# Kernel optimization log

Measured on AMD Instinct MI355X. Metric: run time of the kernel, lower is better.

Reference implementation:

```python
import jax, jax.numpy as jnp
import numpy as np
from jax import lax

FEATURE_NUM = 16
FILTERS = 64
BATCH = 64
WINDOW = 5
T = 2048
SECTORS = 11
D = 256          # embedding dim / number of quantization buckets
DA = 64
VOCAB = 100000
L = T - 3 * WINDOW + 3  # 2036, length after conv->maxpool->conv (all valid, stride 1)
BN_EPS = 1e-5


def _conv1d(x, w):
    # x: [N, C, W], w: [O, I, K], valid padding, stride 1
    return lax.conv_general_dilated(x, w, (1,), 'VALID', dimension_numbers=('NCH', 'OIH', 'NCH'))


def setup_inputs() -> dict:
    key = jax.random.key(0)
    ks = jax.random.split(key, 9)
    x = jax.random.normal(ks[0], (BATCH, 2 * FEATURE_NUM, T), jnp.float32)
    conv1_w = jax.random.normal(ks[1], (FILTERS, 2 * FEATURE_NUM, WINDOW), jnp.float32) * 0.1
    conv1_b = jnp.zeros((FILTERS,), jnp.float32)
    bn_gamma = jnp.ones((FILTERS,), jnp.float32)
    bn_beta = jnp.zeros((FILTERS,), jnp.float32)
    conv2_w = jax.random.normal(ks[2], (1, FILTERS, WINDOW), jnp.float32) * 0.1
    conv2_b = jnp.zeros((1,), jnp.float32)
    emb = jax.random.normal(ks[3], (VOCAB, D), jnp.float32)
    W1 = jax.random.normal(ks[4], (DA, L), jnp.float32)
    W2 = jax.random.normal(ks[5], (DA, 1), jnp.float32)
    lin_w = jax.random.normal(ks[6], (SECTORS, D), jnp.float32) * 0.05
    lin_b = jnp.zeros((SECTORS,), jnp.float32)
    return {'x': x, 'conv1_w': conv1_w, 'conv1_b': conv1_b, 'bn_gamma': bn_gamma,
            'bn_beta': bn_beta, 'conv2_w': conv2_w, 'conv2_b': conv2_b, 'emb': emb,
            'W1': W1, 'W2': W2, 'lin_w': lin_w, 'lin_b': lin_b}


def reference(x, conv1_w, conv1_b, bn_gamma, bn_beta, conv2_w, conv2_b, emb, W1, W2, lin_w, lin_b):
    # conv1 (valid) -> maxpool(k=WINDOW, s=1) -> batchnorm (train-mode batch stats) -> conv2 -> relu
    h = _conv1d(x, conv1_w) + conv1_b[None, :, None]                     # [B, F, T-W+1]
    h = lax.reduce_window(h, -jnp.inf, lax.max, (1, 1, WINDOW), (1, 1, 1), 'VALID')
    mu = jnp.mean(h, axis=(0, 2), keepdims=True)
    var = jnp.mean((h - mu) ** 2, axis=(0, 2), keepdims=True)            # biased, as torch BN train
    h = (h - mu) * lax.rsqrt(var + BN_EPS) * bn_gamma[None, :, None] + bn_beta[None, :, None]
    h = jax.nn.relu(_conv1d(h, conv2_w) + conv2_b[None, :, None])        # [B, 1, L]
    c = jax.nn.sigmoid(h[:, 0, :])                                       # [B, L] in (0,1)
    # embedding_generate: first j with c <= (j+1)/D  <=>  j = ceil(c*D) - 1
    idx = jnp.clip(jnp.ceil(c * D).astype(jnp.int32) - 1, 0, D - 1)      # [B, L]
    e = emb[idx]                                                         # [B, L, D]
    # per-sample attention: A = W2^T tanh(W1 @ out), batched as einsums
    t = jnp.tanh(jnp.einsum('al,bld->bad', W1, e))                       # [B, DA, D]
    A = jnp.einsum('a,bad->bd', W2[:, 0], t)                             # [B, D]
    att = jax.nn.softmax(jnp.einsum('bld,bd->bl', e, A), axis=1)         # [B, L]
    scores = A @ lin_w.T + lin_b                                         # [B, SECTORS]
    return att, scores
```

## Files before the change

### kernel.cpp

```cpp
#include <hip/hip_runtime.h>
#include <hip/hip_bf16.h>
#include <math.h>

#define BATCH 64
#define CIN   32
#define TIN   2048
#define FILT  64
#define WIN   5
#define TP1   2044
#define TP2   2040
#define LOUT  2036
#define DEMB  256
#define DA    64
#define NSEC  11
#define NC    4
#define CS    509
#define TILE_T 252

__global__ __launch_bounds__(256) void k_prep(
    const float* __restrict__ W1, const float* __restrict__ emb,
    const float* __restrict__ w1, float* __restrict__ w1t,
    float* __restrict__ embT, float* __restrict__ w1r, int* __restrict__ count) {
  __shared__ float tl[64 * 65];
  int bk = blockIdx.x;
  const int tid = threadIdx.x;
  if (bk < 64) { count[bk * 256 + tid] = 0; return; }
  bk -= 64;
  if (bk < 32) {
    const int l0 = bk * 64;
    const int lc = tid & 63, rq = tid >> 6;
    for (int a = rq; a < 64; a += 4)
      tl[a * 65 + lc] = (l0 + lc < LOUT) ? W1[a * LOUT + l0 + lc] : 0.f;
    __syncthreads();
    for (int lp = rq; lp < 64; lp += 4)
      if (l0 + lp < LOUT) w1t[(l0 + lp) * 64 + lc] = tl[lc * 65 + lp];
    return;
  }
  bk -= 32;
  if (bk < 16) {
    const int j0 = (bk & 3) * 64, d0 = (bk >> 2) * 64;
    const int c = tid & 63, rq = tid >> 6;
    for (int j = rq; j < 64; j += 4) tl[j * 65 + c] = emb[(j0 + j) * DEMB + d0 + c];
    __syncthreads();
    for (int d = rq; d < 64; d += 4) embT[(d0 + d) * DEMB + j0 + c] = tl[c * 65 + d];
    return;
  }
  bk -= 16;
  {
    int i = bk * 256 + tid;
    int c = i / 320, r = i - c * 320, f = r / 5, k = r - f * 5;
    w1r[i] = w1[f * (CIN * WIN) + c * WIN + k];
  }
}

__global__ __launch_bounds__(256) void k_conv1pool(
    const float* __restrict__ x, const float* __restrict__ w1r,
    const float* __restrict__ b1, float* __restrict__ h2,
    float* __restrict__ bnps, float* __restrict__ bnpq) {
  __shared__ float xl[CIN * 264];
  const int b   = blockIdx.y;
  const int t0  = blockIdx.x * TILE_T;
  const int tid = threadIdx.x;

  for (int i = tid; i < CIN * 264; i += 256) {
    int c = i / 264, o = i - c * 264;
    int gt = t0 + o;
    float v = 0.f;
    if (o < 260 && gt < TIN) v = x[(b * CIN + c) * TIN + gt];
    xl[i] = v;
  }
  __syncthreads();

  const int tg  = tid & 63;
  const int tb  = tg * 4;
  const int wf0 = __builtin_amdgcn_readfirstlane((int)blockIdx.z * 32 + (tid >> 6) * 8);

  float acc[8][4];
#pragma unroll
  for (int ff = 0; ff < 8; ++ff) {
    float bias = b1[wf0 + ff];
    acc[ff][0] = bias; acc[ff][1] = bias; acc[ff][2] = bias; acc[ff][3] = bias;
  }

  for (int c = 0; c < CIN; ++c) {
    float4 xa  = *(const float4*)&xl[c * 264 + tb];
    float4 xb4 = *(const float4*)&xl[c * 264 + tb + 4];
    float xw[8] = {xa.x, xa.y, xa.z, xa.w, xb4.x, xb4.y, xb4.z, xb4.w};
    const float* wr = w1r + c * 320 + wf0 * 5;
#pragma unroll
    for (int ff = 0; ff < 8; ++ff) {
#pragma unroll
      for (int k = 0; k < WIN; ++k) {
        float wv = wr[ff * 5 + k];
        acc[ff][0] = fmaf(xw[k + 0], wv, acc[ff][0]);
        acc[ff][1] = fmaf(xw[k + 1], wv, acc[ff][1]);
        acc[ff][2] = fmaf(xw[k + 2], wv, acc[ff][2]);
        acc[ff][3] = fmaf(xw[k + 3], wv, acc[ff][3]);
      }
    }
  }

  const bool rowvalid = (tg < 63);
  const int blk = b * 9 + blockIdx.x;
#pragma unroll
  for (int ff = 0; ff < 8; ++ff) {
    float n0 = __shfl_down(acc[ff][0], 1);
    float n1 = __shfl_down(acc[ff][1], 1);
    float n2 = __shfl_down(acc[ff][2], 1);
    float n3 = __shfl_down(acc[ff][3], 1);
    float h[8] = {acc[ff][0], acc[ff][1], acc[ff][2], acc[ff][3], n0, n1, n2, n3};
    float o0 = fmaxf(fmaxf(fmaxf(h[0], h[1]), fmaxf(h[2], h[3])), h[4]);
    float o1 = fmaxf(fmaxf(fmaxf(h[1], h[2]), fmaxf(h[3], h[4])), h[5]);
    float o2 = fmaxf(fmaxf(fmaxf(h[2], h[3]), fmaxf(h[4], h[5])), h[6]);
    float o3 = fmaxf(fmaxf(fmaxf(h[3], h[4]), fmaxf(h[5], h[6])), h[7]);
    const int f = wf0 + ff;
    float s = 0.f, q = 0.f;
    const int t2b = t0 + tb;
    if (rowvalid && (t2b + 3 < TP2)) {
      *(float4*)&h2[(b * FILT + f) * TP2 + t2b] = make_float4(o0, o1, o2, o3);
      s = o0 + o1 + o2 + o3;
      q = o0 * o0 + o1 * o1 + o2 * o2 + o3 * o3;
    } else if (rowvalid) {
      float ov[4] = {o0, o1, o2, o3};
#pragma unroll
      for (int j = 0; j < 4; ++j) {
        int t2 = t2b + j;
        if (t2 < TP2) { h2[(b * FILT + f) * TP2 + t2] = ov[j]; s += ov[j]; q += ov[j] * ov[j]; }
      }
    }
#pragma unroll
    for (int off = 32; off > 0; off >>= 1) {
      s += __shfl_down(s, off);
      q += __shfl_down(q, off);
    }
    if (tg == 0) { bnps[blk * FILT + f] = s; bnpq[blk * FILT + f] = q; }
  }
}

__global__ __launch_bounds__(256) void k_bnfin(
    const float* __restrict__ bnps, const float* __restrict__ bnpq,
    const float* __restrict__ gamma, const float* __restrict__ beta,
    const float* __restrict__ w2, const float* __restrict__ b2,
    double* __restrict__ ws2, double* __restrict__ c0p) {
  __shared__ double ls[4 * 64], lq[4 * 64];
  const int tid = threadIdx.x;
  const int f = tid & 63, g = tid >> 6;
  double s = 0.0, q = 0.0;
  for (int blk = g; blk < 576; blk += 4) {
    s += (double)bnps[blk * FILT + f];
    q += (double)bnpq[blk * FILT + f];
  }
  ls[g * 64 + f] = s; lq[g * 64 + f] = q;
  __syncthreads();
  if (tid < 64) {
    s = ls[tid] + ls[64 + tid] + ls[128 + tid] + ls[192 + tid];
    q = lq[tid] + lq[64 + tid] + lq[128 + tid] + lq[192 + tid];
    const double N = (double)(BATCH * TP2);
    double mu  = s / N;
    double var = q / N - mu * mu;
    double sc  = (double)gamma[tid] / sqrt(var + 1e-5);
    double sh  = (double)beta[tid] - mu * sc;
    double wsum = 0.0;
#pragma unroll
    for (int k = 0; k < WIN; ++k) {
      double wv = (double)w2[tid * WIN + k];
      ws2[tid * WIN + k] = sc * wv;
      wsum += wv;
    }
    double part = sh * wsum;
#pragma unroll
    for (int off = 32; off > 0; off >>= 1) part += __shfl_down(part, off);
    if (tid == 0) c0p[0] = part + (double)b2[0];
  }
}

__global__ __launch_bounds__(256) void k_conv2(
    const float* __restrict__ h2, const double* __restrict__ ws2,
    const double* __restrict__ c0p, int* __restrict__ idxp, int* __restrict__ count) {
  __shared__ float hl[FILT * 260];
  __shared__ int hist[DEMB];
  const int b = blockIdx.y;
  const int t0 = blockIdx.x * 256;
  const int tid = threadIdx.x;
  for (int i = tid; i < FILT * 260; i += 256) {
    int f = i / 260, o = i - f * 260;
    int gt = t0 + o;
    hl[i] = (gt < TP2) ? h2[(b * FILT + f) * TP2 + gt] : 0.f;
  }
  hist[tid] = 0;
  __syncthreads();
  const int t = t0 + tid;
  if (t < LOUT) {
    double z = c0p[0];
    for (int f = 0; f < FILT; ++f) {
      const double* wr = ws2 + f * WIN;
      z = fma((double)hl[f * 260 + tid + 0], wr[0], z);
      z = fma((double)hl[f * 260 + tid + 1], wr[1], z);
      z = fma((double)hl[f * 260 + tid + 2], wr[2], z);
      z = fma((double)hl[f * 260 + tid + 3], wr[3], z);
      z = fma((double)hl[f * 260 + tid + 4], wr[4], z);
    }
    z = z > 0.0 ? z : 0.0;
    double c = 1.0 / (1.0 + exp(-z));
    int iv = (int)ceil(c * 256.0) - 1;
    iv = min(max(iv, 0), DEMB - 1);
    idxp[b * LOUT + t] = iv;
    atomicAdd(&hist[iv], 1);
  }
  __syncthreads();
  atomicAdd(&count[b * DEMB + tid], hist[tid]);
}

__global__ __launch_bounds__(256) void k_sbuild(
    const int* __restrict__ idxp, const float* __restrict__ w1t,
    float* __restrict__ Sg) {
  __shared__ float S[DA * 257];
  __shared__ int il[512];
  const int b = blockIdx.y, ch = blockIdx.x;
  const int tid = threadIdx.x;
  for (int i = tid; i < DA * 257; i += 256) S[i] = 0.f;
  const int l0 = ch * CS;
  for (int i = tid; i < CS; i += 256) il[i] = idxp[b * LOUT + l0 + i];
  __syncthreads();
  const int a = tid & 63, w = tid >> 6;
#pragma unroll 4
  for (int li = w; li < CS; li += 4) {
    int j = il[li];
    float v = w1t[(l0 + li) * DA + a];
    atomicAdd(&S[a * 257 + j], v);
  }
  __syncthreads();
  for (int i = tid; i < DA * DEMB; i += 256) {
    int aa = i >> 8, j = i & 255;
    Sg[((b * NC + ch) * DA + aa) * DEMB + j] = S[aa * 257 + j];
  }
}

__global__ __launch_bounds__(256) void k_gemmA(
    const float* __restrict__ Sg, const float* __restrict__ emb,
    const float* __restrict__ W2, float* __restrict__ Avec) {
  __shared__ float Al[16 * 64];
  __shared__ float Bl[16 * 64];
  __shared__ float red[16 * 64];
  const int b = blockIdx.x, c0 = blockIdx.y * 64;
  const int tid = threadIdx.x;
  const int tx = tid & 15, ty = tid >> 4;
  const int sa = tid >> 2, skq = (tid & 3) * 4;
  const int bk = tid >> 4, bseg = tid & 15;
  float acc[4][4] = {{0}};

  for (int kc = 0; kc < 16; ++kc) {
    const int kb = kc * 16;
    float4 v0 = *(const float4*)&Sg[((b * NC + 0) * DA + sa) * DEMB + kb + skq];
    float4 v1 = *(const float4*)&Sg[((b * NC + 1) * DA + sa) * DEMB + kb + skq];
    float4 v2 = *(const float4*)&Sg[((b * NC + 2) * DA + sa) * DEMB + kb + skq];
    float4 v3 = *(const float4*)&Sg[((b * NC + 3) * DA + sa) * DEMB + kb + skq];
    float4 sv = make_float4(v0.x + v1.x + v2.x + v3.x, v0.y + v1.y + v2.y + v3.y,
                            v0.z + v1.z + v2.z + v3.z, v0.w + v1.w + v2.w + v3.w);
    Al[(skq + 0) * 64 + sa] = sv.x;
    Al[(skq + 1) * 64 + sa] = sv.y;
    Al[(skq + 2) * 64 + sa] = sv.z;
    Al[(skq + 3) * 64 + sa] = sv.w;
    float4 e4 = *(const float4*)&emb[(kb + bk) * DEMB + c0 + bseg * 4];
    *(float4*)&Bl[bk * 64 + bseg * 4] = e4;
    __syncthreads();
#pragma unroll
    for (int k = 0; k < 16; ++k) {
      float4 av = *(const float4*)&Al[k * 64 + ty * 4];
      float4 bv = *(const float4*)&Bl[k * 64 + tx * 4];
      acc[0][0] = fmaf(av.x, bv.x, acc[0][0]); acc[0][1] = fmaf(av.x, bv.y, acc[0][1]);
      acc[0][2] = fmaf(av.x, bv.z, acc[0][2]); acc[0][3] = fmaf(av.x, bv.w, acc[0][3]);
      acc[1][0] = fmaf(av.y, bv.x, acc[1][0]); acc[1][1] = fmaf(av.y, bv.y, acc[1][1]);
      acc[1][2] = fmaf(av.y, bv.z, acc[1][2]); acc[1][3] = fmaf(av.y, bv.w, acc[1][3]);
      acc[2][0] = fmaf(av.z, bv.x, acc[2][0]); acc[2][1] = fmaf(av.z, bv.y, acc[2][1]);
      acc[2][2] = fmaf(av.z, bv.z, acc[2][2]); acc[2][3] = fmaf(av.z, bv.w, acc[2][3]);
      acc[3][0] = fmaf(av.w, bv.x, acc[3][0]); acc[3][1] = fmaf(av.w, bv.y, acc[3][1]);
      acc[3][2] = fmaf(av.w, bv.z, acc[3][2]); acc[3][3] = fmaf(av.w, bv.w, acc[3][3]);
    }
    __syncthreads();
  }
  float cs[4] = {0.f, 0.f, 0.f, 0.f};
#pragma unroll
  for (int r = 0; r < 4; ++r) {
    float wv = W2[ty * 4 + r];
#pragma unroll
    for (int j = 0; j < 4; ++j) cs[j] += tanhf(acc[r][j]) * wv;
  }
#pragma unroll
  for (int j = 0; j < 4; ++j) red[ty * 64 + tx * 4 + j] = cs[j];
  __syncthreads();
  if (tid < 64) {
    float s = 0.f;
#pragma unroll
    for (int q = 0; q < 16; ++q) s += red[q * 64 + tid];
    Avec[b * DEMB + c0 + tid] = s;
  }
}

__global__ __launch_bounds__(256) void k_att(
    const float* __restrict__ Avec, const float* __restrict__ embT,
    const int* __restrict__ count, const float* __restrict__ linw,
    const float* __restrict__ linb, const int* __restrict__ idxp,
    float* __restrict__ att, float* __restrict__ scores) {
  __shared__ float Al[DEMB];
  __shared__ float pl[DEMB];
  __shared__ float scratch[4];
  const int b = blockIdx.x, j = threadIdx.x;
  Al[j] = Avec[b * DEMB + j];
  __syncthreads();
  float dot = 0.f;
  for (int d = 0; d < DEMB; ++d) dot = fmaf(embT[d * DEMB + j], Al[d], dot);
  const int cnt = count[b * DEMB + j];
  float v = (cnt > 0) ? dot : -3.4e38f;
#pragma unroll
  for (int off = 32; off > 0; off >>= 1) v = fmaxf(v, __shfl_down(v, off));
  if ((j & 63) == 0) scratch[j >> 6] = v;
  __syncthreads();
  const float m = fmaxf(fmaxf(scratch[0], scratch[1]), fmaxf(scratch[2], scratch[3]));
  __syncthreads();
  float e = (cnt > 0) ? expf(dot - m) : 0.f;
  float zs = e * (float)cnt;
#pragma unroll
  for (int off = 32; off > 0; off >>= 1) zs += __shfl_down(zs, off);
  if ((j & 63) == 0) scratch[j >> 6] = zs;
  __syncthreads();
  const float Z = scratch[0] + scratch[1] + scratch[2] + scratch[3];
  pl[j] = (cnt > 0) ? e / Z : 0.f;
  __syncthreads();
  for (int l = j; l < LOUT; l += 256)
    att[b * LOUT + l] = pl[idxp[b * LOUT + l]];
  for (int s = 0; s < NSEC; ++s) {
    __syncthreads();
    float part = Al[j] * linw[s * DEMB + j];
#pragma unroll
    for (int off = 32; off > 0; off >>= 1) part += __shfl_down(part, off);
    if ((j & 63) == 0) scratch[j >> 6] = part;
    __syncthreads();
    if (j == 0)
      scores[b * NSEC + s] = scratch[0] + scratch[1] + scratch[2] + scratch[3] + linb[s];
  }
}

extern "C" void kernel_launch(void* const* d_in, const int* in_sizes, int n_in,
                              void* d_out, int out_size, void* d_ws, size_t ws_size,
                              hipStream_t stream) {
  const float* x      = (const float*)d_in[0];
  const float* w1     = (const float*)d_in[1];
  const float* b1     = (const float*)d_in[2];
  const float* gamma  = (const float*)d_in[3];
  const float* beta   = (const float*)d_in[4];
  const float* w2     = (const float*)d_in[5];
  const float* b2     = (const float*)d_in[6];
  const float* emb    = (const float*)d_in[7];
  const float* W1     = (const float*)d_in[8];
  const float* W2     = (const float*)d_in[9];
  const float* linw   = (const float*)d_in[10];
  const float* linb   = (const float*)d_in[11];

  char* ws = (char*)d_ws;
  int*    count = (int*)   (ws + 0);
  double* ws2   = (double*)(ws + 65536);
  double* c0p   = (double*)(ws + 68096);
  float*  bnps  = (float*) (ws + 68608);
  float*  bnpq  = (float*) (ws + 216064);
  int*    idxp  = (int*)   (ws + 363520);
  float*  w1t   = (float*) (ws + 884736);
  float*  embT  = (float*) (ws + 1405952);
  float*  Avec  = (float*) (ws + 1668096);
  float*  w1r   = (float*) (ws + 1733632);
  float*  h2    = (float*) (ws + 1774592);
  float*  Sg    = (float*) (ws + 35197952);

  float* att_out    = (float*)d_out;
  float* scores_out = (float*)d_out + BATCH * LOUT;

  k_prep<<<dim3(152), 256, 0, stream>>>(W1, emb, w1, w1t, embT, w1r, count);
  k_conv1pool<<<dim3(9, 64, 2), 256, 0, stream>>>(x, w1r, b1, h2, bnps, bnpq);
  k_bnfin<<<dim3(1), 256, 0, stream>>>(bnps, bnpq, gamma, beta, w2, b2, ws2, c0p);
  k_conv2<<<dim3(8, 64), 256, 0, stream>>>(h2, ws2, c0p, idxp, count);
  k_sbuild<<<dim3(NC, 64), 256, 0, stream>>>(idxp, w1t, Sg);
  k_gemmA<<<dim3(64, 4), 256, 0, stream>>>(Sg, emb, W2, Avec);
  k_att<<<dim3(64), 256, 0, stream>>>(Avec, embT, count, linw, linb, idxp,
                                      att_out, scores_out);
}
```

Measured before the change: 377.0 us.

## Stage conv1 weights in LDS and read input directly from global memory

The conv1+maxpool kernel no longer stages the input tile in shared memory. Each thread now loads its eight input values straight from global memory with float4 reads and a bounds-checked fallback at the edge. The per-block half of the reordered conv1 weights is staged in LDS instead and read as float4 vectors into registers, replacing the scalar global weight loads. This trades input reuse through LDS for cached global reads of overlapping windows, and the 40-element weight array in registers raises register pressure. Index arithmetic is also widened to size_t.

```diff
diff --git a/kernel.cpp b/kernel.cpp
--- a/kernel.cpp
+++ b/kernel.cpp
@@ -57,23 +57,22 @@
     const float* __restrict__ x, const float* __restrict__ w1r,
     const float* __restrict__ b1, float* __restrict__ h2,
     float* __restrict__ bnps, float* __restrict__ bnpq) {
-  __shared__ float xl[CIN * 264];
+  __shared__ float wl[CIN * 160];
   const int b   = blockIdx.y;
   const int t0  = blockIdx.x * TILE_T;
   const int tid = threadIdx.x;
-
-  for (int i = tid; i < CIN * 264; i += 256) {
-    int c = i / 264, o = i - c * 264;
-    int gt = t0 + o;
-    float v = 0.f;
-    if (o < 260 && gt < TIN) v = x[(b * CIN + c) * TIN + gt];
-    xl[i] = v;
-  }
-  __syncthreads();
-
-  const int tg  = tid & 63;
-  const int tb  = tg * 4;
-  const int wf0 = __builtin_amdgcn_readfirstlane((int)blockIdx.z * 32 + (tid >> 6) * 8);
+  const int z   = blockIdx.z;
+
+  for (int i = tid; i < CIN * 160; i += 256) {
+    int c = i / 160, r = i - c * 160;
+    wl[i] = w1r[c * 320 + z * 160 + r];
+  }
+  __syncthreads();
+
+  const int tg   = tid & 63;
+  const int tb   = tg * 4;
+  const int wv40 = (tid >> 6) * 40;
+  const int wf0  = __builtin_amdgcn_readfirstlane(z * 32 + (tid >> 6) * 8);
 
   float acc[8][4];
 #pragma unroll
@@ -82,16 +81,35 @@
     acc[ff][0] = bias; acc[ff][1] = bias; acc[ff][2] = bias; acc[ff][3] = bias;
   }
 
+  const float* xrow = x + (size_t)b * CIN * TIN + t0 + tb;
+  const bool safe = (t0 + tb + 8) <= TIN;
+
   for (int c = 0; c < CIN; ++c) {
-    float4 xa  = *(const float4*)&xl[c * 264 + tb];
-    float4 xb4 = *(const float4*)&xl[c * 264 + tb + 4];
-    float xw[8] = {xa.x, xa.y, xa.z, xa.w, xb4.x, xb4.y, xb4.z, xb4.w};
-    const float* wr = w1r + c * 320 + wf0 * 5;
+    float xw[8];
+    if (safe) {
+      float4 xa = *(const float4*)(xrow + c * TIN);
+      float4 xb = *(const float4*)(xrow + c * TIN + 4);
+      xw[0] = xa.x; xw[1] = xa.y; xw[2] = xa.z; xw[3] = xa.w;
+      xw[4] = xb.x; xw[5] = xb.y; xw[6] = xb.z; xw[7] = xb.w;
+    } else {
+#pragma unroll
+      for (int j = 0; j < 8; ++j) {
+        int gt = t0 + tb + j;
+        xw[j] = (gt < TIN) ? xrow[c * TIN + j] : 0.f;
+      }
+    }
+    float wa[40];
+#pragma unroll
+    for (int q = 0; q < 10; ++q) {
+      float4 wq = *(const float4*)&wl[c * 160 + wv40 + q * 4];
+      wa[q * 4 + 0] = wq.x; wa[q * 4 + 1] = wq.y;
+      wa[q * 4 + 2] = wq.z; wa[q * 4 + 3] = wq.w;
+    }
 #pragma unroll
     for (int ff = 0; ff < 8; ++ff) {
 #pragma unroll
       for (int k = 0; k < WIN; ++k) {
-        float wv = wr[ff * 5 + k];
+        float wv = wa[ff * 5 + k];
         acc[ff][0] = fmaf(xw[k + 0], wv, acc[ff][0]);
         acc[ff][1] = fmaf(xw[k + 1], wv, acc[ff][1]);
         acc[ff][2] = fmaf(xw[k + 2], wv, acc[ff][2]);
@@ -117,7 +135,7 @@
     float s = 0.f, q = 0.f;
     const int t2b = t0 + tb;
     if (rowvalid && (t2b + 3 < TP2)) {
-      *(float4*)&h2[(b * FILT + f) * TP2 + t2b] = make_float4(o0, o1, o2, o3);
+      *(float4*)&h2[((size_t)b * FILT + f) * TP2 + t2b] = make_float4(o0, o1, o2, o3);
       s = o0 + o1 + o2 + o3;
       q = o0 * o0 + o1 * o1 + o2 * o2 + o3 * o3;
     } else if (rowvalid) {
@@ -125,7 +143,7 @@
 #pragma unroll
       for (int j = 0; j < 4; ++j) {
         int t2 = t2b + j;
-        if (t2 < TP2) { h2[(b * FILT + f) * TP2 + t2] = ov[j]; s += ov[j]; q += ov[j] * ov[j]; }
+        if (t2 < TP2) { h2[((size_t)b * FILT + f) * TP2 + t2] = ov[j]; s += ov[j]; q += ov[j] * ov[j]; }
       }
     }
 #pragma unroll
@@ -185,7 +203,7 @@
   for (int i = tid; i < FILT * 260; i += 256) {
     int f = i / 260, o = i - f * 260;
     int gt = t0 + o;
-    hl[i] = (gt < TP2) ? h2[(b * FILT + f) * TP2 + gt] : 0.f;
+    hl[i] = (gt < TP2) ? h2[((size_t)b * FILT + f) * TP2 + gt] : 0.f;
   }
   hist[tid] = 0;
   __syncthreads();
```

New measurement: 368.2 us. 1.02x faster.
